# Kernel optimization log

Measured on AMD Instinct MI355X. Metric: run time of the kernel, lower is better.

## Reference

```python
import jax, jax.numpy as jnp
import numpy as np

EPS = 1e-8


def setup_inputs() -> dict:
    key = jax.random.key(0)
    ks = jax.random.split(key, 9)
    num_queries, num_keys = 8192, 524288
    num_bins, num_freqs = 128, 64
    head_dim = 2 * num_freqs
    return {
        "Q": jax.random.normal(ks[0], (num_queries, head_dim), jnp.float32),
        "K": jax.random.normal(ks[1], (num_keys, head_dim), jnp.float32),
        "reference_angles": jax.random.uniform(ks[2], (num_freqs,), jnp.float32),
        "probes": jax.random.normal(ks[3], (num_bins, head_dim), jnp.float32),
        "k_magnitude_weights": jax.random.normal(ks[4], (num_bins, num_freqs), jnp.float32),
        "k_bias": jax.random.normal(ks[5], (num_bins,), jnp.float32),
        "q_weights_raw": jax.random.normal(ks[6], (num_bins, num_freqs), jnp.float32),
        "q_magnitude_weights": jax.random.normal(ks[7], (num_bins, num_freqs), jnp.float32),
        "q_bias": jax.random.normal(ks[8], (num_bins,), jnp.float32),
    }


def _l2_normalize(x):
    return x / (jnp.linalg.norm(x, axis=-1, keepdims=True) + EPS)


def reference(Q, K, reference_angles, probes, k_magnitude_weights, k_bias,
              q_weights_raw, q_magnitude_weights, q_bias):
    num_bins, head_dim = probes.shape
    num_freqs = head_dim // 2

    # --- shared probe layer: L2-normalize probes then RoPE-rotate by reference angles ---
    p = _l2_normalize(probes)                              # (B, D)
    pc = p.reshape(num_bins, num_freqs, 2)                 # (B, F, 2)
    cos_t = jnp.cos(reference_angles)                      # (F,)
    sin_t = jnp.sin(reference_angles)
    rot_pairs = jnp.stack(
        [pc[..., 0] * cos_t - pc[..., 1] * sin_t,
         pc[..., 0] * sin_t + pc[..., 1] * cos_t], axis=-1)  # (B, F, 2)
    rotated_probes = rot_pairs.reshape(num_bins, head_dim)   # (B, D)

    # --- Key network: dot product + magnitude term + bias (K NOT normalized) ---
    dot_term = K @ rotated_probes.T                                   # (Nk, B)
    K_mag = jnp.sqrt(jnp.sum(K.reshape(-1, num_freqs, 2) ** 2, -1) + EPS)  # (Nk, F)
    k_logits = dot_term + K_mag @ k_magnitude_weights.T + k_bias      # (Nk, B)

    # --- Query network: distance-based scoring on L2-normalized Q ---
    Qn = _l2_normalize(Q)                                  # (Nq, D)
    Qf = Qn.reshape(-1, num_freqs, 2)                      # (Nq, F, 2)
    err = rot_pairs[None, :, :, :] - Qf[:, None, :, :]     # (Nq, B, F, 2)
    dist = jnp.sqrt(jnp.sum(err ** 2, -1) + EPS)           # (Nq, B, F)
    Q_mag = jnp.sqrt(jnp.sum(Qf ** 2, -1) + EPS)           # (Nq, F)
    eff_w = -jax.nn.softplus(q_weights_raw)                # (B, F), negative weights
    dist_term = jnp.sum(dist * eff_w[None, :, :], -1)      # (Nq, B)
    q_logits = dist_term + Q_mag @ q_magnitude_weights.T + q_bias  # (Nq, B)

    return k_logits, q_logits
```

## Files before the change

kernel.cpp:

```cpp
#include <hip/hip_runtime.h>
#include <hip/hip_bf16.h>
#include <math.h>

#define NQ 8192
#define NK 524288
#define NB 128
#define NF 64
#define ND 128
#define EPSF 1e-8f

using bf16x8 = __attribute__((ext_vector_type(8))) short;
using f32x4  = __attribute__((ext_vector_type(4))) float;

__device__ __forceinline__ unsigned short f2bf(float x) {
    union { float f; unsigned int u; } v; v.f = x;
    unsigned int u = v.u;
    return (unsigned short)((u + 0x7FFFu + ((u >> 16) & 1u)) >> 16);
}

__device__ __forceinline__ int frag_index(int k, int b) {
    int kc = k >> 5, kl = k & 31, quad = kl >> 3, j = kl & 7;
    int nt = b >> 4, ln = (quad << 4) | (b & 15);
    return ((kc * 8 + nt) * 64 + ln) * 8 + j;
}

__global__ void prep_kernel(const float* __restrict__ angles,
                            const float* __restrict__ probes,
                            const float* __restrict__ kmw,
                            const float* __restrict__ qwr,
                            const float* __restrict__ qmw,
                            unsigned short* __restrict__ Bfrag,
                            float4* __restrict__ Ppack) {
    int t = threadIdx.x;
    int b = t >> 1;
    int half = t & 1;
    const float* pr = probes + b * ND;
    float ss = 0.f;
    for (int i = 0; i < ND; i += 4) {
        float4 v = *(const float4*)(pr + i);
        ss += v.x * v.x + v.y * v.y + v.z * v.z + v.w * v.w;
    }
    float scale = 1.f / (sqrtf(ss) + EPSF);
    int f0 = half * 32;
    for (int f = f0; f < f0 + 32; ++f) {
        float p0 = pr[2 * f] * scale;
        float p1 = pr[2 * f + 1] * scale;
        float c = cosf(angles[f]);
        float s = sinf(angles[f]);
        float rx = p0 * c - p1 * s;
        float ry = p0 * s + p1 * c;
        float x = qwr[b * NF + f];
        float sp = fmaxf(x, 0.f) + log1pf(expf(-fabsf(x)));
        float ew = -sp;
        float qw = qmw[b * NF + f];
        Ppack[b * NF + f] = make_float4(rx, ry, ew, qw);
        Bfrag[frag_index(2 * f, b)]     = f2bf(rx);
        Bfrag[frag_index(2 * f + 1, b)] = f2bf(ry);
        Bfrag[frag_index(128 + f, b)]   = f2bf(kmw[b * NF + f]);
    }
}

__global__ __launch_bounds__(256, 2)
void k_gemm(const float* __restrict__ Kg,
            const unsigned short* __restrict__ Bfrag_g,
            const float* __restrict__ k_bias,
            float* __restrict__ out) {
    __shared__ unsigned short Alds[64 * 200];
    __shared__ unsigned short Blds[6 * 8 * 64 * 8];
    int t = threadIdx.x;

    {
        const uint4* src = (const uint4*)Bfrag_g;
        uint4* dst = (uint4*)Blds;
        #pragma unroll
        for (int i = 0; i < 12; ++i) dst[i * 256 + t] = src[i * 256 + t];
    }
    int rowbase = blockIdx.x * 64;
    #pragma unroll
    for (int i = 0; i < 8; ++i) {
        int idx = i * 256 + t;
        int row = idx >> 5;
        int c = idx & 31;
        float4 v = *(const float4*)(Kg + (size_t)(rowbase + row) * ND + c * 4);
        unsigned int lo = (unsigned int)f2bf(v.x) | ((unsigned int)f2bf(v.y) << 16);
        unsigned int hi = (unsigned int)f2bf(v.z) | ((unsigned int)f2bf(v.w) << 16);
        *(unsigned int*)&Alds[row * 200 + c * 4]     = lo;
        *(unsigned int*)&Alds[row * 200 + c * 4 + 2] = hi;
        float m0 = sqrtf(v.x * v.x + v.y * v.y + EPSF);
        float m1 = sqrtf(v.z * v.z + v.w * v.w + EPSF);
        *(unsigned int*)&Alds[row * 200 + 128 + c * 2] =
            (unsigned int)f2bf(m0) | ((unsigned int)f2bf(m1) << 16);
    }
    __syncthreads();

    int lane = t & 63;
    int w = t >> 6;
    int m = lane & 15, quad = lane >> 4;
    f32x4 acc[8];
    #pragma unroll
    for (int i = 0; i < 8; ++i) acc[i] = (f32x4){0.f, 0.f, 0.f, 0.f};

    #pragma unroll
    for (int kc = 0; kc < 6; ++kc) {
        bf16x8 a = *(const bf16x8*)&Alds[(w * 16 + m) * 200 + kc * 32 + quad * 8];
        #pragma unroll
        for (int nt = 0; nt < 8; ++nt) {
            bf16x8 bb = *(const bf16x8*)&Blds[((kc * 8 + nt) * 64 + lane) * 8];
            acc[nt] = __builtin_amdgcn_mfma_f32_16x16x32_bf16(a, bb, acc[nt], 0, 0, 0);
        }
    }
    int orow = rowbase + w * 16 + quad * 4;
    #pragma unroll
    for (int nt = 0; nt < 8; ++nt) {
        int col = nt * 16 + m;
        float bias = k_bias[col];
        #pragma unroll
        for (int r = 0; r < 4; ++r)
            out[(size_t)(orow + r) * NB + col] = acc[nt][r] + bias;
    }
}

__global__ __launch_bounds__(256, 3)
void q_kernel(const float* __restrict__ Qg,
              const float4* __restrict__ Ppack,
              const float* __restrict__ q_bias,
              float* __restrict__ outq) {
    __shared__ float Plds[32 * 260];
    __shared__ float Qlds[8 * 256];
    int t = threadIdx.x;
    int bg = blockIdx.x & 3;
    int rb = blockIdx.x >> 2;

    #pragma unroll
    for (int i = 0; i < 8; ++i) {
        int idx = i * 256 + t;
        int lb = idx >> 6, f = idx & 63;
        float4 v = Ppack[(bg * 32 + lb) * 64 + f];
        *(float4*)&Plds[lb * 260 + f * 4] = v;
    }

    int r = t >> 5;
    int c = t & 31;
    int lb = c;
    float bias = q_bias[bg * 32 + lb];

    for (int chunk = 0; chunk < 4; ++chunk) {
        __syncthreads();
        int grow = rb * 32 + chunk * 8 + r;
        float4 v = *(const float4*)(Qg + (size_t)grow * ND + c * 4);
        float ss = v.x * v.x + v.y * v.y + v.z * v.z + v.w * v.w;
        #pragma unroll
        for (int msk = 1; msk < 32; msk <<= 1) ss += __shfl_xor(ss, msk);
        float inv = 1.f / (sqrtf(ss) + EPSF);
        float qx0 = v.x * inv, qy0 = v.y * inv;
        float qx1 = v.z * inv, qy1 = v.w * inv;
        float qm0 = sqrtf(qx0 * qx0 + qy0 * qy0 + EPSF);
        float qm1 = sqrtf(qx1 * qx1 + qy1 * qy1 + EPSF);
        *(float4*)&Qlds[r * 256 + c * 8]     = make_float4(qx0, qy0, qm0, 0.f);
        *(float4*)&Qlds[r * 256 + c * 8 + 4] = make_float4(qx1, qy1, qm1, 0.f);
        __syncthreads();

        float acc = 0.f;
        #pragma unroll 8
        for (int f = 0; f < 64; ++f) {
            float4 P  = *(const float4*)&Plds[lb * 260 + f * 4];
            float4 Qp = *(const float4*)&Qlds[r * 256 + f * 4];
            float dx = P.x - Qp.x, dy = P.y - Qp.y;
            float d = sqrtf(fmaf(dx, dx, fmaf(dy, dy, EPSF)));
            acc = fmaf(P.z, d, acc);
            acc = fmaf(P.w, Qp.z, acc);
        }
        outq[(size_t)grow * NB + bg * 32 + lb] = acc + bias;
    }
}

extern "C" void kernel_launch(void* const* d_in, const int* in_sizes, int n_in,
                              void* d_out, int out_size, void* d_ws, size_t ws_size,
                              hipStream_t stream) {
    const float* Q      = (const float*)d_in[0];
    const float* K      = (const float*)d_in[1];
    const float* angles = (const float*)d_in[2];
    const float* probes = (const float*)d_in[3];
    const float* kmw    = (const float*)d_in[4];
    const float* kb     = (const float*)d_in[5];
    const float* qwr    = (const float*)d_in[6];
    const float* qmw    = (const float*)d_in[7];
    const float* qb     = (const float*)d_in[8];
    float* out = (float*)d_out;

    unsigned short* Bfrag = (unsigned short*)d_ws;
    float4* Ppack = (float4*)((char*)d_ws + 65536);

    prep_kernel<<<1, 256, 0, stream>>>(angles, probes, kmw, qwr, qmw, Bfrag, Ppack);
    k_gemm<<<NK / 64, 256, 0, stream>>>(K, Bfrag, kb, out);
    q_kernel<<<1024, 256, 0, stream>>>(Q, Ppack, qb, out + (size_t)NK * NB);
}
```

Baseline: 562.8 us.

## Load K fragments directly to registers, loop tiles per block, register-tile Q kernel

The K GEMM no longer stages A through LDS. Each lane loads its MFMA fragment straight from global memory, converts it to bf16 and computes the magnitude columns in registers. Each block now handles four 64-row tiles so the B-fragment LDS load is amortized, and the launch bounds are raised for occupancy. The Q kernel is restructured so each thread computes a 2-row by 4-bin register tile with a transposed probe layout, raising reuse per LDS load, at the cost of uncoalesced per-lane K loads and some redundant reads of K for the magnitude fragments.

Result: slower. 746.6 us (+32.6%).

```diff
diff --git a/kernel.cpp b/kernel.cpp
--- a/kernel.cpp
+++ b/kernel.cpp
@@ -53,19 +53,18 @@
         float sp = fmaxf(x, 0.f) + log1pf(expf(-fabsf(x)));
         float ew = -sp;
         float qw = qmw[b * NF + f];
-        Ppack[b * NF + f] = make_float4(rx, ry, ew, qw);
+        Ppack[f * NB + b] = make_float4(rx, ry, ew, qw);
         Bfrag[frag_index(2 * f, b)]     = f2bf(rx);
         Bfrag[frag_index(2 * f + 1, b)] = f2bf(ry);
         Bfrag[frag_index(128 + f, b)]   = f2bf(kmw[b * NF + f]);
     }
 }
 
-__global__ __launch_bounds__(256, 2)
+__global__ __launch_bounds__(256, 3)
 void k_gemm(const float* __restrict__ Kg,
             const unsigned short* __restrict__ Bfrag_g,
             const float* __restrict__ k_bias,
             float* __restrict__ out) {
-    __shared__ unsigned short Alds[64 * 200];
     __shared__ unsigned short Blds[6 * 8 * 64 * 8];
     int t = threadIdx.x;
 
@@ -75,58 +74,84 @@
         #pragma unroll
         for (int i = 0; i < 12; ++i) dst[i * 256 + t] = src[i * 256 + t];
     }
-    int rowbase = blockIdx.x * 64;
-    #pragma unroll
-    for (int i = 0; i < 8; ++i) {
-        int idx = i * 256 + t;
-        int row = idx >> 5;
-        int c = idx & 31;
-        float4 v = *(const float4*)(Kg + (size_t)(rowbase + row) * ND + c * 4);
-        unsigned int lo = (unsigned int)f2bf(v.x) | ((unsigned int)f2bf(v.y) << 16);
-        unsigned int hi = (unsigned int)f2bf(v.z) | ((unsigned int)f2bf(v.w) << 16);
-        *(unsigned int*)&Alds[row * 200 + c * 4]     = lo;
-        *(unsigned int*)&Alds[row * 200 + c * 4 + 2] = hi;
-        float m0 = sqrtf(v.x * v.x + v.y * v.y + EPSF);
-        float m1 = sqrtf(v.z * v.z + v.w * v.w + EPSF);
-        *(unsigned int*)&Alds[row * 200 + 128 + c * 2] =
-            (unsigned int)f2bf(m0) | ((unsigned int)f2bf(m1) << 16);
-    }
     __syncthreads();
 
-    int lane = t & 63;
-    int w = t >> 6;
-    int m = lane & 15, quad = lane >> 4;
-    f32x4 acc[8];
-    #pragma unroll
-    for (int i = 0; i < 8; ++i) acc[i] = (f32x4){0.f, 0.f, 0.f, 0.f};
-
-    #pragma unroll
-    for (int kc = 0; kc < 6; ++kc) {
-        bf16x8 a = *(const bf16x8*)&Alds[(w * 16 + m) * 200 + kc * 32 + quad * 8];
+    int lane = t & 63, w = t >> 6;
+    int m = lane & 15, q = lane >> 4;
+
+    #pragma unroll 1
+    for (int tt = 0; tt < 4; ++tt) {
+        int row = blockIdx.x * 256 + tt * 64 + w * 16 + m;
+        const float* Kr = Kg + (size_t)row * ND;
+
+        float4 va[8];
+        #pragma unroll
+        for (int kc = 0; kc < 4; ++kc) {
+            va[2 * kc]     = *(const float4*)(Kr + kc * 32 + q * 8);
+            va[2 * kc + 1] = *(const float4*)(Kr + kc * 32 + q * 8 + 4);
+        }
+        float4 vm[8];
+        #pragma unroll
+        for (int h = 0; h < 2; ++h)
+            #pragma unroll
+            for (int jj = 0; jj < 4; ++jj)
+                vm[h * 4 + jj] = *(const float4*)(Kr + h * 64 + q * 16 + jj * 4);
+
+        bf16x8 a[6];
+        #pragma unroll
+        for (int kc = 0; kc < 4; ++kc) {
+            union { bf16x8 v; unsigned short s[8]; } u;
+            float4 v0 = va[2 * kc], v1 = va[2 * kc + 1];
+            u.s[0] = f2bf(v0.x); u.s[1] = f2bf(v0.y);
+            u.s[2] = f2bf(v0.z); u.s[3] = f2bf(v0.w);
+            u.s[4] = f2bf(v1.x); u.s[5] = f2bf(v1.y);
+            u.s[6] = f2bf(v1.z); u.s[7] = f2bf(v1.w);
+            a[kc] = u.v;
+        }
+        #pragma unroll
+        for (int h = 0; h < 2; ++h) {
+            union { bf16x8 v; unsigned short s[8]; } u;
+            #pragma unroll
+            for (int jj = 0; jj < 4; ++jj) {
+                float4 v = vm[h * 4 + jj];
+                u.s[2 * jj]     = f2bf(sqrtf(v.x * v.x + v.y * v.y + EPSF));
+                u.s[2 * jj + 1] = f2bf(sqrtf(v.z * v.z + v.w * v.w + EPSF));
+            }
+            a[4 + h] = u.v;
+        }
+
+        f32x4 acc[8];
+        #pragma unroll
+        for (int i = 0; i < 8; ++i) acc[i] = (f32x4){0.f, 0.f, 0.f, 0.f};
+
+        #pragma unroll
+        for (int kc = 0; kc < 6; ++kc) {
+            #pragma unroll
+            for (int nt = 0; nt < 8; ++nt) {
+                bf16x8 bb = *(const bf16x8*)&Blds[((kc * 8 + nt) * 64 + lane) * 8];
+                acc[nt] = __builtin_amdgcn_mfma_f32_16x16x32_bf16(a[kc], bb, acc[nt], 0, 0, 0);
+            }
+        }
+
+        int orow = blockIdx.x * 256 + tt * 64 + w * 16 + q * 4;
         #pragma unroll
         for (int nt = 0; nt < 8; ++nt) {
-            bf16x8 bb = *(const bf16x8*)&Blds[((kc * 8 + nt) * 64 + lane) * 8];
-            acc[nt] = __builtin_amdgcn_mfma_f32_16x16x32_bf16(a, bb, acc[nt], 0, 0, 0);
-        }
-    }
-    int orow = rowbase + w * 16 + quad * 4;
-    #pragma unroll
-    for (int nt = 0; nt < 8; ++nt) {
-        int col = nt * 16 + m;
-        float bias = k_bias[col];
-        #pragma unroll
-        for (int r = 0; r < 4; ++r)
-            out[(size_t)(orow + r) * NB + col] = acc[nt][r] + bias;
-    }
-}
-
-__global__ __launch_bounds__(256, 3)
+            int col = nt * 16 + m;
+            float bias = k_bias[col];
+            #pragma unroll
+            for (int r = 0; r < 4; ++r)
+                out[(size_t)(orow + r) * NB + col] = acc[nt][r] + bias;
+        }
+    }
+}
+
+__global__ __launch_bounds__(256, 2)
 void q_kernel(const float* __restrict__ Qg,
               const float4* __restrict__ Ppack,
               const float* __restrict__ q_bias,
               float* __restrict__ outq) {
-    __shared__ float Plds[32 * 260];
-    __shared__ float Qlds[8 * 256];
+    __shared__ float4 Plds[64 * 32];
+    __shared__ float  Qlds[64 * 130];
     int t = threadIdx.x;
     int bg = blockIdx.x & 3;
     int rb = blockIdx.x >> 2;
@@ -134,43 +159,53 @@
     #pragma unroll
     for (int i = 0; i < 8; ++i) {
         int idx = i * 256 + t;
-        int lb = idx >> 6, f = idx & 63;
-        float4 v = Ppack[(bg * 32 + lb) * 64 + f];
-        *(float4*)&Plds[lb * 260 + f * 4] = v;
-    }
-
-    int r = t >> 5;
-    int c = t & 31;
-    int lb = c;
-    float bias = q_bias[bg * 32 + lb];
-
-    for (int chunk = 0; chunk < 4; ++chunk) {
-        __syncthreads();
-        int grow = rb * 32 + chunk * 8 + r;
-        float4 v = *(const float4*)(Qg + (size_t)grow * ND + c * 4);
+        int f = idx >> 5, bl = idx & 31;
+        Plds[idx] = Ppack[f * NB + bg * 32 + bl];
+    }
+    #pragma unroll
+    for (int i = 0; i < 8; ++i) {
+        int r = i * 8 + (t >> 5);
+        int c = t & 31;
+        float4 v = *(const float4*)(Qg + (size_t)(rb * 64 + r) * ND + c * 4);
         float ss = v.x * v.x + v.y * v.y + v.z * v.z + v.w * v.w;
         #pragma unroll
         for (int msk = 1; msk < 32; msk <<= 1) ss += __shfl_xor(ss, msk);
         float inv = 1.f / (sqrtf(ss) + EPSF);
-        float qx0 = v.x * inv, qy0 = v.y * inv;
-        float qx1 = v.z * inv, qy1 = v.w * inv;
-        float qm0 = sqrtf(qx0 * qx0 + qy0 * qy0 + EPSF);
-        float qm1 = sqrtf(qx1 * qx1 + qy1 * qy1 + EPSF);
-        *(float4*)&Qlds[r * 256 + c * 8]     = make_float4(qx0, qy0, qm0, 0.f);
-        *(float4*)&Qlds[r * 256 + c * 8 + 4] = make_float4(qx1, qy1, qm1, 0.f);
-        __syncthreads();
-
-        float acc = 0.f;
-        #pragma unroll 8
-        for (int f = 0; f < 64; ++f) {
-            float4 P  = *(const float4*)&Plds[lb * 260 + f * 4];
-            float4 Qp = *(const float4*)&Qlds[r * 256 + f * 4];
-            float dx = P.x - Qp.x, dy = P.y - Qp.y;
-            float d = sqrtf(fmaf(dx, dx, fmaf(dy, dy, EPSF)));
-            acc = fmaf(P.z, d, acc);
-            acc = fmaf(P.w, Qp.z, acc);
-        }
-        outq[(size_t)grow * NB + bg * 32 + lb] = acc + bias;
+        *(float2*)&Qlds[r * 130 + c * 4]     = make_float2(v.x * inv, v.y * inv);
+        *(float2*)&Qlds[r * 130 + c * 4 + 2] = make_float2(v.z * inv, v.w * inv);
+    }
+    __syncthreads();
+
+    int lane = t & 63, w = t >> 6;
+    int rp = lane >> 3, bo = lane & 7;
+    int r0 = w * 16 + rp * 2, r1 = r0 + 1;
+
+    float acc[4][2] = {};
+    #pragma unroll 8
+    for (int f = 0; f < 64; ++f) {
+        float2 q0 = *(const float2*)&Qlds[r0 * 130 + 2 * f];
+        float2 q1 = *(const float2*)&Qlds[r1 * 130 + 2 * f];
+        float qm0 = sqrtf(fmaf(q0.x, q0.x, fmaf(q0.y, q0.y, EPSF)));
+        float qm1 = sqrtf(fmaf(q1.x, q1.x, fmaf(q1.y, q1.y, EPSF)));
+        #pragma unroll
+        for (int k = 0; k < 4; ++k) {
+            float4 P = Plds[f * 32 + k * 8 + bo];
+            float dx0 = P.x - q0.x, dy0 = P.y - q0.y;
+            float d0 = sqrtf(fmaf(dx0, dx0, fmaf(dy0, dy0, EPSF)));
+            acc[k][0] = fmaf(P.z, d0, acc[k][0]);
+            acc[k][0] = fmaf(P.w, qm0, acc[k][0]);
+            float dx1 = P.x - q1.x, dy1 = P.y - q1.y;
+            float d1 = sqrtf(fmaf(dx1, dx1, fmaf(dy1, dy1, EPSF)));
+            acc[k][1] = fmaf(P.z, d1, acc[k][1]);
+            acc[k][1] = fmaf(P.w, qm1, acc[k][1]);
+        }
+    }
+    #pragma unroll
+    for (int k = 0; k < 4; ++k) {
+        int col = bg * 32 + k * 8 + bo;
+        float bias = q_bias[col];
+        outq[(size_t)(rb * 64 + r0) * NB + col] = acc[k][0] + bias;
+        outq[(size_t)(rb * 64 + r1) * NB + col] = acc[k][1] + bias;
     }
 }
 
@@ -192,6 +227,6 @@
     float4* Ppack = (float4*)((char*)d_ws + 65536);
 
     prep_kernel<<<1, 256, 0, stream>>>(angles, probes, kmw, qwr, qmw, Bfrag, Ppack);
-    k_gemm<<<NK / 64, 256, 0, stream>>>(K, Bfrag, kb, out);
-    q_kernel<<<1024, 256, 0, stream>>>(Q, Ppack, qb, out + (size_t)NK * NB);
-}
+    k_gemm<<<NK / 256, 256, 0, stream>>>(K, Bfrag, kb, out);
+    q_kernel<<<(NQ / 64) * 4, 256, 0, stream>>>(Q, Ppack, qb, out + (size_t)NK * NB);
+}
```
